# Performance work log

Measured on AMD Instinct MI355X. Metric: run time of the kernel, lower is better.

## Reference

```python
import jax, jax.numpy as jnp
import numpy as np

N_NODES = 50000


def graph_conv(h, src, dst, W, b, num_nodes):
    """GCN-style conv: transform node features, then sum messages over edges.
    h: [N, Din], W: [Din, Dout] -> out: [N, Dout].
    """
    m = (h @ W)[src]                                   # [E, Dout] per-edge messages
    agg = jax.ops.segment_sum(m, dst, num_segments=num_nodes)  # [N, Dout]
    return agg + b


def setup_inputs() -> dict:
    key = jax.random.key(0)
    ks = jax.random.split(key, 8)
    N, E, D = N_NODES, 800000, 128
    s = 1.0 / np.sqrt(2 * D)
    return {
        "node_feature": jax.random.normal(ks[0], (N, D), jnp.float32),
        "H_prev": jax.random.normal(ks[1], (N, D), jnp.float32),
        "edge_index": jax.random.randint(ks[2], (2, E), 0, N, jnp.int32),
        "W_main": jax.random.normal(ks[3], (D, D), jnp.float32) / np.sqrt(D),
        "b_main": jnp.zeros((D,), jnp.float32),
        "W_z": jax.random.normal(ks[4], (2 * D, D), jnp.float32) * s,
        "b_z": jnp.zeros((D,), jnp.float32),
        "W_r": jax.random.normal(ks[5], (2 * D, D), jnp.float32) * s,
        "b_r": jnp.zeros((D,), jnp.float32),
        "W_h": jax.random.normal(ks[6], (2 * D, D), jnp.float32) * s,
        "b_h": jnp.zeros((D,), jnp.float32),
    }


def reference(node_feature, H_prev, edge_index, W_main, b_main,
              W_z, b_z, W_r, b_r, W_h, b_h):
    N = node_feature.shape[0]
    src, dst = edge_index[0], edge_index[1]
    # main message-passing layer + post-layer activation (ReLU)
    X = jax.nn.relu(graph_conv(node_feature, src, dst, W_main, b_main, N))
    # GRU-gated graph convolutions
    cat_zr = jnp.concatenate([X, H_prev], axis=1)       # [N, 2D]
    Z = jax.nn.sigmoid(graph_conv(cat_zr, src, dst, W_z, b_z, N))
    R = jax.nn.sigmoid(graph_conv(cat_zr, src, dst, W_r, b_r, N))
    cat_h = jnp.concatenate([X, R * H_prev], axis=1)
    H_tilde = jnp.tanh(graph_conv(cat_h, src, dst, W_h, b_h, N))
    H_out = Z * H_prev + (1.0 - Z) * H_tilde
    return H_out
```

## Files before the change

kernel.cpp:

```cpp
#include <hip/hip_runtime.h>
#include <hip/hip_fp16.h>
#include <math.h>

typedef _Float16 f16;
typedef f16 f16x2 __attribute__((ext_vector_type(2)));
typedef f16 f16x4 __attribute__((ext_vector_type(4)));
typedef f16 f16x8 __attribute__((ext_vector_type(8)));
typedef float f32x4_t __attribute__((ext_vector_type(4)));

__device__ __forceinline__ float sigmoidf(float x) {
  return 1.0f / (1.0f + __expf(-x));
}

__global__ void zero_ints(int* __restrict__ p, int n) {
  int i = blockIdx.x * blockDim.x + threadIdx.x;
  if (i < n) p[i] = 0;
}

__global__ void count_kernel(const int* __restrict__ dst, int* __restrict__ cnt, int E) {
  int e = blockIdx.x * blockDim.x + threadIdx.x;
  if (e < E) atomicAdd(&cnt[dst[e]], 1);
}

__global__ void scan_kernel(const int* __restrict__ cnt, int* __restrict__ off,
                            int* __restrict__ cur, int n) {
  __shared__ int wsum[16];
  __shared__ int carry_s;
  const int tid = threadIdx.x;
  const int lane = tid & 63, wid = tid >> 6;
  if (tid == 0) carry_s = 0;
  __syncthreads();
  for (int base = 0; base < n; base += 1024) {
    int i = base + tid;
    int v = (i < n) ? cnt[i] : 0;
    int x = v;
    #pragma unroll
    for (int d = 1; d < 64; d <<= 1) {
      int y = __shfl_up(x, d);
      if (lane >= d) x += y;
    }
    if (lane == 63) wsum[wid] = x;
    __syncthreads();
    if (wid == 0) {
      int ws = (lane < 16) ? wsum[lane] : 0;
      #pragma unroll
      for (int d = 1; d < 16; d <<= 1) {
        int y = __shfl_up(ws, d);
        if (lane >= d) ws += y;
      }
      if (lane < 16) wsum[lane] = ws;
    }
    __syncthreads();
    int carry = carry_s;
    int woff = (wid > 0) ? wsum[wid - 1] : 0;
    int incl = x + woff;
    int excl = carry + incl - v;
    if (i < n) { off[i] = excl; cur[i] = excl; }
    __syncthreads();
    if (tid == 1023) carry_s = carry + incl;
    __syncthreads();
  }
  if (threadIdx.x == 0) { off[n] = carry_s; cur[n] = carry_s; }
}

__global__ void fill_kernel(const int* __restrict__ src, const int* __restrict__ dst,
                            int* __restrict__ cur, int* __restrict__ esrc, int E) {
  int e = blockIdx.x * blockDim.x + threadIdx.x;
  if (e < E) {
    int d = dst[e];
    int p = atomicAdd(&cur[d], 1);
    esrc[p] = src[e];
  }
}

__global__ void wtrans_all(const float* __restrict__ Wm, const float* __restrict__ Wz,
                           const float* __restrict__ Wr, const float* __restrict__ Wh,
                           f16* __restrict__ WtM, f16* __restrict__ WtZR,
                           f16* __restrict__ WtH) {
  __shared__ float tile[32][33];
  const float* W;
  f16* O;
  int K;
  switch (blockIdx.z) {
    case 0: W = Wm; O = WtM; K = 128; break;
    case 1: W = Wz; O = WtZR; K = 256; break;
    case 2: W = Wr; O = WtZR + 128 * 256; K = 256; break;
    default: W = Wh; O = WtH; K = 256; break;
  }
  int bk = blockIdx.x * 32, bn = blockIdx.y * 32;
  if (bk >= K) return;
  int tx = threadIdx.x, ty = threadIdx.y;
  #pragma unroll
  for (int i = 0; i < 4; ++i)
    tile[ty + 8 * i][tx] = W[(size_t)(bk + ty + 8 * i) * 128 + bn + tx];
  __syncthreads();
  #pragma unroll
  for (int i = 0; i < 4; ++i)
    O[(size_t)(bn + ty + 8 * i) * K + bk + tx] = (f16)tile[tx][ty + 8 * i];
}

template <int TERMS, int A0F32, int A1F32>
__global__ __launch_bounds__(256) void gemm_mfma(
    const void* __restrict__ A0v, const void* __restrict__ A1v,
    const f16* __restrict__ Wt, f16* __restrict__ C, int ldc, int N) {
  constexpr int KTOT = TERMS * 128;
  __shared__ __align__(16) f16 As[128][72];
  __shared__ __align__(16) f16 Bs[128][72];
  const int tid = threadIdx.x;
  const int l = tid & 63, w = tid >> 6;
  const int wr = (w >> 1) * 64, wc = (w & 1) * 64;
  const int fr = l & 15;
  const int kg = (l >> 4) * 8;
  const int brow = blockIdx.x * 128;
  const int coff = blockIdx.y * 128;

  f32x4_t acc[4][4];
  #pragma unroll
  for (int m = 0; m < 4; ++m)
    #pragma unroll
    for (int n = 0; n < 4; ++n) acc[m][n] = (f32x4_t)0.0f;

  #pragma unroll
  for (int kk = 0; kk < KTOT; kk += 64) {
    const bool sel1 = (TERMS == 2) && (kk >= 128);
    const void* Av = sel1 ? A1v : A0v;
    const bool srcF32 = sel1 ? (A1F32 != 0) : (A0F32 != 0);
    const int klocal = sel1 ? (kk - 128) : kk;

    __syncthreads();
    #pragma unroll
    for (int p = 0; p < 4; ++p) {
      int g = tid + 256 * p;
      int row = g >> 3;
      int kc = (g & 7) * 8;
      int grow = brow + row;
      f16x8 v = {};
      if (grow < N) {
        if (srcF32) {
          const float* Ap = (const float*)Av + (size_t)grow * 128 + klocal + kc;
          float4 u0 = *(const float4*)Ap;
          float4 u1 = *(const float4*)(Ap + 4);
          v[0] = (f16)u0.x; v[1] = (f16)u0.y; v[2] = (f16)u0.z; v[3] = (f16)u0.w;
          v[4] = (f16)u1.x; v[5] = (f16)u1.y; v[6] = (f16)u1.z; v[7] = (f16)u1.w;
        } else {
          v = *(const f16x8*)((const f16*)Av + (size_t)grow * 128 + klocal + kc);
        }
      }
      *(f16x8*)&As[row][kc] = v;
    }
    #pragma unroll
    for (int p = 0; p < 4; ++p) {
      int g = tid + 256 * p;
      int c = g >> 3;
      int kc = (g & 7) * 8;
      *(f16x8*)&Bs[c][kc] = *(const f16x8*)&Wt[(size_t)(coff + c) * KTOT + kk + kc];
    }
    __syncthreads();

    #pragma unroll
    for (int ks = 0; ks < 2; ++ks) {
      f16x8 a[4], b[4];
      #pragma unroll
      for (int m = 0; m < 4; ++m)
        a[m] = *(const f16x8*)&As[wr + m * 16 + fr][ks * 32 + kg];
      #pragma unroll
      for (int n = 0; n < 4; ++n)
        b[n] = *(const f16x8*)&Bs[wc + n * 16 + fr][ks * 32 + kg];
      #pragma unroll
      for (int m = 0; m < 4; ++m)
        #pragma unroll
        for (int n = 0; n < 4; ++n)
          acc[m][n] = __builtin_amdgcn_mfma_f32_16x16x32_f16(a[m], b[n], acc[m][n], 0, 0, 0);
    }
  }

  const int rbase = (l >> 4) * 4;
  if (brow + 128 <= N) {
    #pragma unroll
    for (int m = 0; m < 4; ++m) {
      int row0 = brow + wr + m * 16 + rbase;
      #pragma unroll
      for (int n = 0; n < 4; ++n) {
        int col = coff + wc + n * 16 + fr;
        #pragma unroll
        for (int r = 0; r < 4; ++r)
          C[(size_t)(row0 + r) * ldc + col] = (f16)acc[m][n][r];
      }
    }
  } else {
    #pragma unroll
    for (int m = 0; m < 4; ++m) {
      int row0 = brow + wr + m * 16 + rbase;
      #pragma unroll
      for (int n = 0; n < 4; ++n) {
        int col = coff + wc + n * 16 + fr;
        #pragma unroll
        for (int r = 0; r < 4; ++r)
          if (row0 + r < N) C[(size_t)(row0 + r) * ldc + col] = (f16)acc[m][n][r];
      }
    }
  }
}

__global__ void gather_relu(const f16* __restrict__ T, const int* __restrict__ off,
                            const int* __restrict__ esrc, const float* __restrict__ bias,
                            f16* __restrict__ X, int N) {
  int w = (blockIdx.x * blockDim.x + threadIdx.x) >> 6;
  int lane = threadIdx.x & 63;
  if (w >= N) return;
  int beg = off[w], end = off[w + 1];
  float ax = 0.f, ay = 0.f;
  int j = beg;
  for (; j + 4 <= end; j += 4) {
    int r0 = esrc[j], r1 = esrc[j + 1], r2 = esrc[j + 2], r3 = esrc[j + 3];
    f16x2 v0 = *(const f16x2*)&T[(size_t)r0 * 128 + lane * 2];
    f16x2 v1 = *(const f16x2*)&T[(size_t)r1 * 128 + lane * 2];
    f16x2 v2 = *(const f16x2*)&T[(size_t)r2 * 128 + lane * 2];
    f16x2 v3 = *(const f16x2*)&T[(size_t)r3 * 128 + lane * 2];
    ax += ((float)v0.x + (float)v1.x) + ((float)v2.x + (float)v3.x);
    ay += ((float)v0.y + (float)v1.y) + ((float)v2.y + (float)v3.y);
  }
  for (; j < end; ++j) {
    f16x2 v = *(const f16x2*)&T[(size_t)esrc[j] * 128 + lane * 2];
    ax += (float)v.x; ay += (float)v.y;
  }
  float2 b = *(const float2*)&bias[lane * 2];
  f16x2 o;
  o.x = (f16)fmaxf(ax + b.x, 0.f);
  o.y = (f16)fmaxf(ay + b.y, 0.f);
  *(f16x2*)&X[(size_t)w * 128 + lane * 2] = o;
}

__global__ void gather_zr(const f16* __restrict__ P, const int* __restrict__ off,
                          const int* __restrict__ esrc, const float* __restrict__ bz,
                          const float* __restrict__ br, const float* __restrict__ H,
                          f16* __restrict__ Z, f16* __restrict__ G, int N) {
  int w = (blockIdx.x * blockDim.x + threadIdx.x) >> 6;
  int lane = threadIdx.x & 63;
  if (w >= N) return;
  int beg = off[w], end = off[w + 1];
  float a0 = 0.f, a1 = 0.f, a2 = 0.f, a3 = 0.f;
  int j = beg;
  for (; j + 4 <= end; j += 4) {
    int r0 = esrc[j], r1 = esrc[j + 1], r2 = esrc[j + 2], r3 = esrc[j + 3];
    f16x4 v0 = *(const f16x4*)&P[(size_t)r0 * 256 + lane * 4];
    f16x4 v1 = *(const f16x4*)&P[(size_t)r1 * 256 + lane * 4];
    f16x4 v2 = *(const f16x4*)&P[(size_t)r2 * 256 + lane * 4];
    f16x4 v3 = *(const f16x4*)&P[(size_t)r3 * 256 + lane * 4];
    a0 += ((float)v0.x + (float)v1.x) + ((float)v2.x + (float)v3.x);
    a1 += ((float)v0.y + (float)v1.y) + ((float)v2.y + (float)v3.y);
    a2 += ((float)v0.z + (float)v1.z) + ((float)v2.z + (float)v3.z);
    a3 += ((float)v0.w + (float)v1.w) + ((float)v2.w + (float)v3.w);
  }
  for (; j < end; ++j) {
    f16x4 v = *(const f16x4*)&P[(size_t)esrc[j] * 256 + lane * 4];
    a0 += (float)v.x; a1 += (float)v.y; a2 += (float)v.z; a3 += (float)v.w;
  }
  if (lane < 32) {
    int c = lane * 4;
    float4 b = *(const float4*)&bz[c];
    f16x4 o;
    o.x = (f16)sigmoidf(a0 + b.x);
    o.y = (f16)sigmoidf(a1 + b.y);
    o.z = (f16)sigmoidf(a2 + b.z);
    o.w = (f16)sigmoidf(a3 + b.w);
    *(f16x4*)&Z[(size_t)w * 128 + c] = o;
  } else {
    int c = (lane - 32) * 4;
    float4 b = *(const float4*)&br[c];
    float4 h = *(const float4*)&H[(size_t)w * 128 + c];
    f16x4 o;
    o.x = (f16)(sigmoidf(a0 + b.x) * h.x);
    o.y = (f16)(sigmoidf(a1 + b.y) * h.y);
    o.z = (f16)(sigmoidf(a2 + b.z) * h.z);
    o.w = (f16)(sigmoidf(a3 + b.w) * h.w);
    *(f16x4*)&G[(size_t)w * 128 + c] = o;
  }
}

__global__ void gather_out(const f16* __restrict__ T, const int* __restrict__ off,
                           const int* __restrict__ esrc, const float* __restrict__ bh,
                           const f16* __restrict__ Z, const float* __restrict__ H,
                           float* __restrict__ out, int N) {
  int w = (blockIdx.x * blockDim.x + threadIdx.x) >> 6;
  int lane = threadIdx.x & 63;
  if (w >= N) return;
  int beg = off[w], end = off[w + 1];
  float ax = 0.f, ay = 0.f;
  int j = beg;
  for (; j + 4 <= end; j += 4) {
    int r0 = esrc[j], r1 = esrc[j + 1], r2 = esrc[j + 2], r3 = esrc[j + 3];
    f16x2 v0 = *(const f16x2*)&T[(size_t)r0 * 128 + lane * 2];
    f16x2 v1 = *(const f16x2*)&T[(size_t)r1 * 128 + lane * 2];
    f16x2 v2 = *(const f16x2*)&T[(size_t)r2 * 128 + lane * 2];
    f16x2 v3 = *(const f16x2*)&T[(size_t)r3 * 128 + lane * 2];
    ax += ((float)v0.x + (float)v1.x) + ((float)v2.x + (float)v3.x);
    ay += ((float)v0.y + (float)v1.y) + ((float)v2.y + (float)v3.y);
  }
  for (; j < end; ++j) {
    f16x2 v = *(const f16x2*)&T[(size_t)esrc[j] * 128 + lane * 2];
    ax += (float)v.x; ay += (float)v.y;
  }
  float2 b = *(const float2*)&bh[lane * 2];
  float h0 = tanhf(ax + b.x), h1 = tanhf(ay + b.y);
  size_t q = (size_t)w * 128 + lane * 2;
  f16x2 zv = *(const f16x2*)&Z[q];
  float2 h = *(const float2*)&H[q];
  float z0 = (float)zv.x, z1 = (float)zv.y;
  float2 o;
  o.x = z0 * h.x + (1.0f - z0) * h0;
  o.y = z1 * h.y + (1.0f - z1) * h1;
  *(float2*)&out[q] = o;
}


extern "C" void kernel_launch(void* const* d_in, const int* in_sizes, int n_in,
                              void* d_out, int out_size, void* d_ws, size_t ws_size,
                              hipStream_t stream) {
  const float* nf = (const float*)d_in[0];
  const float* H  = (const float*)d_in[1];
  const int*   ei = (const int*)d_in[2];
  const float* Wm = (const float*)d_in[3];
  const float* bm = (const float*)d_in[4];
  const float* Wz = (const float*)d_in[5];
  const float* bz = (const float*)d_in[6];
  const float* Wr = (const float*)d_in[7];
  const float* br = (const float*)d_in[8];
  const float* Wh = (const float*)d_in[9];
  const float* bh = (const float*)d_in[10];
  float* out = (float*)d_out;

  const int N = in_sizes[0] / 128;
  const int E = in_sizes[2] / 2;
  const int* src = ei;
  const int* dst = ei + E;

  char* ws = (char*)d_ws;
  size_t o = 0;
  auto alloc = [&](size_t bytes) {
    char* p = ws + o;
    o = (o + bytes + 511) & ~(size_t)511;
    return p;
  };
  int* cnt    = (int*)alloc((size_t)N * 4);
  int* off    = (int*)alloc((size_t)(N + 1) * 4);
  int* cur    = (int*)alloc((size_t)(N + 1) * 4);
  int* esrc   = (int*)alloc((size_t)E * 4);
  f16* WtM    = (f16*)alloc((size_t)128 * 128 * 2);
  f16* WtZR   = (f16*)alloc((size_t)256 * 256 * 2);
  f16* WtH    = (f16*)alloc((size_t)128 * 256 * 2);
  f16* Tm     = (f16*)alloc((size_t)N * 128 * 2);
  f16* Pzr    = (f16*)alloc((size_t)N * 256 * 2);
  f16* Th     = (f16*)alloc((size_t)N * 128 * 2);
  f16* X      = (f16*)alloc((size_t)N * 128 * 2);
  f16* G      = (f16*)alloc((size_t)N * 128 * 2);
  f16* Zh     = (f16*)alloc((size_t)N * 128 * 2);

  zero_ints<<<(N + 255) / 256, 256, 0, stream>>>(cnt, N);
  count_kernel<<<(E + 255) / 256, 256, 0, stream>>>(dst, cnt, E);
  scan_kernel<<<1, 1024, 0, stream>>>(cnt, off, cur, N);
  fill_kernel<<<(E + 255) / 256, 256, 0, stream>>>(src, dst, cur, esrc, E);

  wtrans_all<<<dim3(8, 4, 4), dim3(32, 8), 0, stream>>>(Wm, Wz, Wr, Wh, WtM, WtZR, WtH);

  const int gblk = (N * 64 + 255) / 256;
  const int mblk = (N + 127) / 128;

  gemm_mfma<1, 1, 0><<<dim3(mblk, 1), 256, 0, stream>>>(nf, nullptr, WtM, Tm, 128, N);
  gather_relu<<<gblk, 256, 0, stream>>>(Tm, off, esrc, bm, X, N);

  gemm_mfma<2, 0, 1><<<dim3(mblk, 2), 256, 0, stream>>>(X, H, WtZR, Pzr, 256, N);
  gather_zr<<<gblk, 256, 0, stream>>>(Pzr, off, esrc, bz, br, H, Zh, G, N);

  gemm_mfma<2, 0, 0><<<dim3(mblk, 1), 256, 0, stream>>>(X, G, WtH, Th, 128, N);
  gather_out<<<gblk, 256, 0, stream>>>(Th, off, esrc, bh, Zh, H, out, N);
}
```

Before: 334.4 us.

## Aggregate before transforming, fuse activations into GEMM epilogues, parallelize CSR scan

Uses linearity to reorder each graph conv from transform-then-gather to gather-then-transform, so neighbor sums run on packed f16 inputs and the bias and activations (ReLU, sigmoid, tanh and the GRU blend) move into the MFMA GEMM epilogues. The separate gather kernels with fused activations go away, and the buffers for node features, Z and the output are aliased to reuse memory. The single-block CSR prefix scan becomes a three-kernel multi-block scan, and edge sources are stored as pre-shifted byte offsets to save address arithmetic. The cost is an extra pack kernel that converts node features and H to f16, plus ordering constraints from the buffer aliasing; there are also small rounding differences because sums are now taken before the matmul.

```diff
diff --git a/kernel.cpp b/kernel.cpp
--- a/kernel.cpp
+++ b/kernel.cpp
@@ -22,55 +22,84 @@
   if (e < E) atomicAdd(&cnt[dst[e]], 1);
 }
 
-__global__ void scan_kernel(const int* __restrict__ cnt, int* __restrict__ off,
-                            int* __restrict__ cur, int n) {
+__global__ __launch_bounds__(1024) void scan_local(const int* __restrict__ cnt,
+                                                   int* __restrict__ off,
+                                                   int* __restrict__ psum, int n) {
   __shared__ int wsum[16];
-  __shared__ int carry_s;
-  const int tid = threadIdx.x;
-  const int lane = tid & 63, wid = tid >> 6;
-  if (tid == 0) carry_s = 0;
-  __syncthreads();
-  for (int base = 0; base < n; base += 1024) {
-    int i = base + tid;
-    int v = (i < n) ? cnt[i] : 0;
-    int x = v;
-    #pragma unroll
-    for (int d = 1; d < 64; d <<= 1) {
-      int y = __shfl_up(x, d);
-      if (lane >= d) x += y;
-    }
-    if (lane == 63) wsum[wid] = x;
-    __syncthreads();
-    if (wid == 0) {
-      int ws = (lane < 16) ? wsum[lane] : 0;
-      #pragma unroll
-      for (int d = 1; d < 16; d <<= 1) {
-        int y = __shfl_up(ws, d);
-        if (lane >= d) ws += y;
-      }
-      if (lane < 16) wsum[lane] = ws;
-    }
-    __syncthreads();
-    int carry = carry_s;
-    int woff = (wid > 0) ? wsum[wid - 1] : 0;
-    int incl = x + woff;
-    int excl = carry + incl - v;
-    if (i < n) { off[i] = excl; cur[i] = excl; }
-    __syncthreads();
-    if (tid == 1023) carry_s = carry + incl;
-    __syncthreads();
-  }
-  if (threadIdx.x == 0) { off[n] = carry_s; cur[n] = carry_s; }
+  const int tid = threadIdx.x, lane = tid & 63, wid = tid >> 6;
+  int i = blockIdx.x * 1024 + tid;
+  int v = (i < n) ? cnt[i] : 0;
+  int x = v;
+  #pragma unroll
+  for (int d = 1; d < 64; d <<= 1) { int y = __shfl_up(x, d); if (lane >= d) x += y; }
+  if (lane == 63) wsum[wid] = x;
+  __syncthreads();
+  if (wid == 0) {
+    int ws = (lane < 16) ? wsum[lane] : 0;
+    #pragma unroll
+    for (int d = 1; d < 16; d <<= 1) { int y = __shfl_up(ws, d); if (lane >= d) ws += y; }
+    if (lane < 16) wsum[lane] = ws;
+  }
+  __syncthreads();
+  int excl = x - v + (wid ? wsum[wid - 1] : 0);
+  if (i < n) off[i] = excl;
+  if (tid == 1023) psum[blockIdx.x] = wsum[15];
+}
+
+__global__ __launch_bounds__(1024) void scan_carry(int* __restrict__ psum,
+                                                   int* __restrict__ off,
+                                                   int* __restrict__ cur, int nb, int n) {
+  __shared__ int wsum[16];
+  const int tid = threadIdx.x, lane = tid & 63, wid = tid >> 6;
+  int v = (tid < nb) ? psum[tid] : 0;
+  int x = v;
+  #pragma unroll
+  for (int d = 1; d < 64; d <<= 1) { int y = __shfl_up(x, d); if (lane >= d) x += y; }
+  if (lane == 63) wsum[wid] = x;
+  __syncthreads();
+  if (wid == 0) {
+    int ws = (lane < 16) ? wsum[lane] : 0;
+    #pragma unroll
+    for (int d = 1; d < 16; d <<= 1) { int y = __shfl_up(ws, d); if (lane >= d) ws += y; }
+    if (lane < 16) wsum[lane] = ws;
+  }
+  __syncthreads();
+  int excl = x - v + (wid ? wsum[wid - 1] : 0);
+  if (tid < nb) psum[tid] = excl;
+  if (tid == 1023) { off[n] = wsum[15]; cur[n] = wsum[15]; }
+}
+
+__global__ __launch_bounds__(1024) void scan_add(int* __restrict__ off, int* __restrict__ cur,
+                                                 const int* __restrict__ psum, int n) {
+  int i = blockIdx.x * 1024 + threadIdx.x;
+  if (i < n) {
+    int t = off[i] + psum[blockIdx.x];
+    off[i] = t;
+    cur[i] = t;
+  }
 }
 
 __global__ void fill_kernel(const int* __restrict__ src, const int* __restrict__ dst,
-                            int* __restrict__ cur, int* __restrict__ esrc, int E) {
+                            int* __restrict__ cur, int* __restrict__ eoff, int E) {
   int e = blockIdx.x * blockDim.x + threadIdx.x;
   if (e < E) {
     int d = dst[e];
     int p = atomicAdd(&cur[d], 1);
-    esrc[p] = src[e];
-  }
+    eoff[p] = src[e] << 8;
+  }
+}
+
+__global__ void pack_nfh(const float* __restrict__ nf, const float* __restrict__ H,
+                         f16* __restrict__ P0, int N) {
+  int gid = blockIdx.x * blockDim.x + threadIdx.x;
+  int w = gid >> 6;
+  if (w >= N) return;
+  int lane = threadIdx.x & 63;
+  const float* S = (lane < 32) ? nf : H;
+  int c = (lane & 31) * 4;
+  float4 u = *(const float4*)&S[(size_t)w * 128 + c];
+  f16x4 o = {(f16)u.x, (f16)u.y, (f16)u.z, (f16)u.w};
+  *(f16x4*)&P0[(size_t)w * 256 + (lane < 32 ? 0 : 128) + c] = o;
 }
 
 __global__ void wtrans_all(const float* __restrict__ Wm, const float* __restrict__ Wz,
@@ -99,10 +128,68 @@
     O[(size_t)(bn + ty + 8 * i) * K + bk + tx] = (f16)tile[tx][ty + 8 * i];
 }
 
-template <int TERMS, int A0F32, int A1F32>
+template <int COLS>
+__global__ __launch_bounds__(256) void gather(const f16* __restrict__ P,
+                                              const int* __restrict__ off,
+                                              const int* __restrict__ eoff,
+                                              f16* __restrict__ O, int N) {
+  int gid = blockIdx.x * blockDim.x + threadIdx.x;
+  int w = __builtin_amdgcn_readfirstlane(gid >> 6);
+  if (w >= N) return;
+  const int lane = threadIdx.x & 63;
+  const int beg = off[w], end = off[w + 1];
+  const char* base = (const char*)P;
+  int j = beg;
+  if constexpr (COLS == 256) {
+    const int lb = lane * 8;
+    float a0 = 0.f, a1 = 0.f, a2 = 0.f, a3 = 0.f;
+    for (; j + 8 <= end; j += 8) {
+      f16x4 v[8];
+      #pragma unroll
+      for (int u = 0; u < 8; ++u) {
+        int bo = (eoff[j + u] << 1) + lb;
+        v[u] = *(const f16x4*)(base + bo);
+      }
+      #pragma unroll
+      for (int u = 0; u < 8; ++u) {
+        a0 += (float)v[u].x; a1 += (float)v[u].y;
+        a2 += (float)v[u].z; a3 += (float)v[u].w;
+      }
+    }
+    for (; j < end; ++j) {
+      int bo = (eoff[j] << 1) + lb;
+      f16x4 v = *(const f16x4*)(base + bo);
+      a0 += (float)v.x; a1 += (float)v.y; a2 += (float)v.z; a3 += (float)v.w;
+    }
+    f16x4 o = {(f16)a0, (f16)a1, (f16)a2, (f16)a3};
+    *(f16x4*)&O[(size_t)w * 256 + lane * 4] = o;
+  } else {
+    const int lb = lane * 4;
+    float a0 = 0.f, a1 = 0.f;
+    for (; j + 8 <= end; j += 8) {
+      f16x2 v[8];
+      #pragma unroll
+      for (int u = 0; u < 8; ++u)
+        v[u] = *(const f16x2*)(base + eoff[j + u] + lb);
+      #pragma unroll
+      for (int u = 0; u < 8; ++u) { a0 += (float)v[u].x; a1 += (float)v[u].y; }
+    }
+    for (; j < end; ++j) {
+      f16x2 v = *(const f16x2*)(base + eoff[j] + lb);
+      a0 += (float)v.x; a1 += (float)v.y;
+    }
+    f16x2 o = {(f16)a0, (f16)a1};
+    *(f16x2*)&O[(size_t)w * 128 + lane * 2] = o;
+  }
+}
+
+template <int TERMS, int EPI>
 __global__ __launch_bounds__(256) void gemm_mfma(
-    const void* __restrict__ A0v, const void* __restrict__ A1v,
-    const f16* __restrict__ Wt, f16* __restrict__ C, int ldc, int N) {
+    const f16* __restrict__ A0, int lda0, const f16* __restrict__ A1, int lda1,
+    const f16* __restrict__ Wt,
+    const float* __restrict__ b0, const float* __restrict__ b1,
+    const float* __restrict__ H, const f16* __restrict__ Zh,
+    f16* __restrict__ O0, f16* __restrict__ O1, float* __restrict__ Ofp, int N) {
   constexpr int KTOT = TERMS * 128;
   __shared__ __align__(16) f16 As[128][72];
   __shared__ __align__(16) f16 Bs[128][72];
@@ -123,9 +210,9 @@
   #pragma unroll
   for (int kk = 0; kk < KTOT; kk += 64) {
     const bool sel1 = (TERMS == 2) && (kk >= 128);
-    const void* Av = sel1 ? A1v : A0v;
-    const bool srcF32 = sel1 ? (A1F32 != 0) : (A0F32 != 0);
-    const int klocal = sel1 ? (kk - 128) : kk;
+    const f16* __restrict__ A = sel1 ? A1 : A0;
+    const int lda = sel1 ? lda1 : lda0;
+    const int klocal = kk & 127;
 
     __syncthreads();
     #pragma unroll
@@ -135,17 +222,7 @@
       int kc = (g & 7) * 8;
       int grow = brow + row;
       f16x8 v = {};
-      if (grow < N) {
-        if (srcF32) {
-          const float* Ap = (const float*)Av + (size_t)grow * 128 + klocal + kc;
-          float4 u0 = *(const float4*)Ap;
-          float4 u1 = *(const float4*)(Ap + 4);
-          v[0] = (f16)u0.x; v[1] = (f16)u0.y; v[2] = (f16)u0.z; v[3] = (f16)u0.w;
-          v[4] = (f16)u1.x; v[5] = (f16)u1.y; v[6] = (f16)u1.z; v[7] = (f16)u1.w;
-        } else {
-          v = *(const f16x8*)((const f16*)Av + (size_t)grow * 128 + klocal + kc);
-        }
-      }
+      if (grow < N) v = *(const f16x8*)&A[(size_t)grow * lda + klocal + kc];
       *(f16x8*)&As[row][kc] = v;
     }
     #pragma unroll
@@ -175,142 +252,56 @@
   }
 
   const int rbase = (l >> 4) * 4;
-  if (brow + 128 <= N) {
-    #pragma unroll
-    for (int m = 0; m < 4; ++m) {
-      int row0 = brow + wr + m * 16 + rbase;
-      #pragma unroll
-      for (int n = 0; n < 4; ++n) {
-        int col = coff + wc + n * 16 + fr;
+  #pragma unroll
+  for (int m = 0; m < 4; ++m) {
+    int row0 = brow + wr + m * 16 + rbase;
+    #pragma unroll
+    for (int n = 0; n < 4; ++n) {
+      int colL = wc + n * 16 + fr;
+      if (EPI == 0) {
+        float bias = b0[colL];
         #pragma unroll
-        for (int r = 0; r < 4; ++r)
-          C[(size_t)(row0 + r) * ldc + col] = (f16)acc[m][n][r];
+        for (int r = 0; r < 4; ++r) {
+          int row = row0 + r;
+          if (row < N)
+            O0[(size_t)row * 128 + colL] = (f16)fmaxf(acc[m][n][r] + bias, 0.f);
+        }
+      } else if (EPI == 1) {
+        if (coff == 0) {
+          float bias = b0[colL];
+          #pragma unroll
+          for (int r = 0; r < 4; ++r) {
+            int row = row0 + r;
+            if (row < N)
+              O0[(size_t)row * 128 + colL] = (f16)sigmoidf(acc[m][n][r] + bias);
+          }
+        } else {
+          float bias = b1[colL];
+          #pragma unroll
+          for (int r = 0; r < 4; ++r) {
+            int row = row0 + r;
+            if (row < N) {
+              float g = sigmoidf(acc[m][n][r] + bias) * H[(size_t)row * 128 + colL];
+              O1[(size_t)row * 128 + colL] = (f16)g;
+            }
+          }
+        }
+      } else {
+        float bias = b0[colL];
+        #pragma unroll
+        for (int r = 0; r < 4; ++r) {
+          int row = row0 + r;
+          if (row < N) {
+            size_t q = (size_t)row * 128 + colL;
+            float ht = tanhf(acc[m][n][r] + bias);
+            float z = (float)Zh[q];
+            float h = H[q];
+            Ofp[q] = z * h + (1.0f - z) * ht;
+          }
+        }
       }
     }
-  } else {
-    #pragma unroll
-    for (int m = 0; m < 4; ++m) {
-      int row0 = brow + wr + m * 16 + rbase;
-      #pragma unroll
-      for (int n = 0; n < 4; ++n) {
-        int col = coff + wc + n * 16 + fr;
-        #pragma unroll
-        for (int r = 0; r < 4; ++r)
-          if (row0 + r < N) C[(size_t)(row0 + r) * ldc + col] = (f16)acc[m][n][r];
-      }
-    }
-  }
-}
-
-__global__ void gather_relu(const f16* __restrict__ T, const int* __restrict__ off,
-                            const int* __restrict__ esrc, const float* __restrict__ bias,
-                            f16* __restrict__ X, int N) {
-  int w = (blockIdx.x * blockDim.x + threadIdx.x) >> 6;
-  int lane = threadIdx.x & 63;
-  if (w >= N) return;
-  int beg = off[w], end = off[w + 1];
-  float ax = 0.f, ay = 0.f;
-  int j = beg;
-  for (; j + 4 <= end; j += 4) {
-    int r0 = esrc[j], r1 = esrc[j + 1], r2 = esrc[j + 2], r3 = esrc[j + 3];
-    f16x2 v0 = *(const f16x2*)&T[(size_t)r0 * 128 + lane * 2];
-    f16x2 v1 = *(const f16x2*)&T[(size_t)r1 * 128 + lane * 2];
-    f16x2 v2 = *(const f16x2*)&T[(size_t)r2 * 128 + lane * 2];
-    f16x2 v3 = *(const f16x2*)&T[(size_t)r3 * 128 + lane * 2];
-    ax += ((float)v0.x + (float)v1.x) + ((float)v2.x + (float)v3.x);
-    ay += ((float)v0.y + (float)v1.y) + ((float)v2.y + (float)v3.y);
-  }
-  for (; j < end; ++j) {
-    f16x2 v = *(const f16x2*)&T[(size_t)esrc[j] * 128 + lane * 2];
-    ax += (float)v.x; ay += (float)v.y;
-  }
-  float2 b = *(const float2*)&bias[lane * 2];
-  f16x2 o;
-  o.x = (f16)fmaxf(ax + b.x, 0.f);
-  o.y = (f16)fmaxf(ay + b.y, 0.f);
-  *(f16x2*)&X[(size_t)w * 128 + lane * 2] = o;
-}
-
-__global__ void gather_zr(const f16* __restrict__ P, const int* __restrict__ off,
-                          const int* __restrict__ esrc, const float* __restrict__ bz,
-                          const float* __restrict__ br, const float* __restrict__ H,
-                          f16* __restrict__ Z, f16* __restrict__ G, int N) {
-  int w = (blockIdx.x * blockDim.x + threadIdx.x) >> 6;
-  int lane = threadIdx.x & 63;
-  if (w >= N) return;
-  int beg = off[w], end = off[w + 1];
-  float a0 = 0.f, a1 = 0.f, a2 = 0.f, a3 = 0.f;
-  int j = beg;
-  for (; j + 4 <= end; j += 4) {
-    int r0 = esrc[j], r1 = esrc[j + 1], r2 = esrc[j + 2], r3 = esrc[j + 3];
-    f16x4 v0 = *(const f16x4*)&P[(size_t)r0 * 256 + lane * 4];
-    f16x4 v1 = *(const f16x4*)&P[(size_t)r1 * 256 + lane * 4];
-    f16x4 v2 = *(const f16x4*)&P[(size_t)r2 * 256 + lane * 4];
-    f16x4 v3 = *(const f16x4*)&P[(size_t)r3 * 256 + lane * 4];
-    a0 += ((float)v0.x + (float)v1.x) + ((float)v2.x + (float)v3.x);
-    a1 += ((float)v0.y + (float)v1.y) + ((float)v2.y + (float)v3.y);
-    a2 += ((float)v0.z + (float)v1.z) + ((float)v2.z + (float)v3.z);
-    a3 += ((float)v0.w + (float)v1.w) + ((float)v2.w + (float)v3.w);
-  }
-  for (; j < end; ++j) {
-    f16x4 v = *(const f16x4*)&P[(size_t)esrc[j] * 256 + lane * 4];
-    a0 += (float)v.x; a1 += (float)v.y; a2 += (float)v.z; a3 += (float)v.w;
-  }
-  if (lane < 32) {
-    int c = lane * 4;
-    float4 b = *(const float4*)&bz[c];
-    f16x4 o;
-    o.x = (f16)sigmoidf(a0 + b.x);
-    o.y = (f16)sigmoidf(a1 + b.y);
-    o.z = (f16)sigmoidf(a2 + b.z);
-    o.w = (f16)sigmoidf(a3 + b.w);
-    *(f16x4*)&Z[(size_t)w * 128 + c] = o;
-  } else {
-    int c = (lane - 32) * 4;
-    float4 b = *(const float4*)&br[c];
-    float4 h = *(const float4*)&H[(size_t)w * 128 + c];
-    f16x4 o;
-    o.x = (f16)(sigmoidf(a0 + b.x) * h.x);
-    o.y = (f16)(sigmoidf(a1 + b.y) * h.y);
-    o.z = (f16)(sigmoidf(a2 + b.z) * h.z);
-    o.w = (f16)(sigmoidf(a3 + b.w) * h.w);
-    *(f16x4*)&G[(size_t)w * 128 + c] = o;
-  }
-}
-
-__global__ void gather_out(const f16* __restrict__ T, const int* __restrict__ off,
-                           const int* __restrict__ esrc, const float* __restrict__ bh,
-                           const f16* __restrict__ Z, const float* __restrict__ H,
-                           float* __restrict__ out, int N) {
-  int w = (blockIdx.x * blockDim.x + threadIdx.x) >> 6;
-  int lane = threadIdx.x & 63;
-  if (w >= N) return;
-  int beg = off[w], end = off[w + 1];
-  float ax = 0.f, ay = 0.f;
-  int j = beg;
-  for (; j + 4 <= end; j += 4) {
-    int r0 = esrc[j], r1 = esrc[j + 1], r2 = esrc[j + 2], r3 = esrc[j + 3];
-    f16x2 v0 = *(const f16x2*)&T[(size_t)r0 * 128 + lane * 2];
-    f16x2 v1 = *(const f16x2*)&T[(size_t)r1 * 128 + lane * 2];
-    f16x2 v2 = *(const f16x2*)&T[(size_t)r2 * 128 + lane * 2];
-    f16x2 v3 = *(const f16x2*)&T[(size_t)r3 * 128 + lane * 2];
-    ax += ((float)v0.x + (float)v1.x) + ((float)v2.x + (float)v3.x);
-    ay += ((float)v0.y + (float)v1.y) + ((float)v2.y + (float)v3.y);
-  }
-  for (; j < end; ++j) {
-    f16x2 v = *(const f16x2*)&T[(size_t)esrc[j] * 128 + lane * 2];
-    ax += (float)v.x; ay += (float)v.y;
-  }
-  float2 b = *(const float2*)&bh[lane * 2];
-  float h0 = tanhf(ax + b.x), h1 = tanhf(ay + b.y);
-  size_t q = (size_t)w * 128 + lane * 2;
-  f16x2 zv = *(const f16x2*)&Z[q];
-  float2 h = *(const float2*)&H[q];
-  float z0 = (float)zv.x, z1 = (float)zv.y;
-  float2 o;
-  o.x = z0 * h.x + (1.0f - z0) * h0;
-  o.y = z1 * h.y + (1.0f - z1) * h1;
-  *(float2*)&out[q] = o;
+  }
 }
 
 
@@ -342,36 +333,48 @@
     o = (o + bytes + 511) & ~(size_t)511;
     return p;
   };
+  const int nb = (N + 1023) / 1024;
   int* cnt    = (int*)alloc((size_t)N * 4);
   int* off    = (int*)alloc((size_t)(N + 1) * 4);
   int* cur    = (int*)alloc((size_t)(N + 1) * 4);
-  int* esrc   = (int*)alloc((size_t)E * 4);
+  int* eoff   = (int*)alloc((size_t)E * 4);
+  int* psum   = (int*)alloc((size_t)nb * 4);
   f16* WtM    = (f16*)alloc((size_t)128 * 128 * 2);
   f16* WtZR   = (f16*)alloc((size_t)256 * 256 * 2);
   f16* WtH    = (f16*)alloc((size_t)128 * 256 * 2);
-  f16* Tm     = (f16*)alloc((size_t)N * 128 * 2);
-  f16* Pzr    = (f16*)alloc((size_t)N * 256 * 2);
-  f16* Th     = (f16*)alloc((size_t)N * 128 * 2);
+  f16* P0     = (f16*)alloc((size_t)N * 256 * 2);
   f16* X      = (f16*)alloc((size_t)N * 128 * 2);
+  f16* AX     = (f16*)alloc((size_t)N * 128 * 2);
   f16* G      = (f16*)alloc((size_t)N * 128 * 2);
-  f16* Zh     = (f16*)alloc((size_t)N * 128 * 2);
+  f16* AP0    = (f16*)d_out;
+  f16* Zh     = X;
+  f16* AG     = P0;
 
   zero_ints<<<(N + 255) / 256, 256, 0, stream>>>(cnt, N);
   count_kernel<<<(E + 255) / 256, 256, 0, stream>>>(dst, cnt, E);
-  scan_kernel<<<1, 1024, 0, stream>>>(cnt, off, cur, N);
-  fill_kernel<<<(E + 255) / 256, 256, 0, stream>>>(src, dst, cur, esrc, E);
+  scan_local<<<nb, 1024, 0, stream>>>(cnt, off, psum, N);
+  scan_carry<<<1, 1024, 0, stream>>>(psum, off, cur, nb, N);
+  scan_add<<<nb, 1024, 0, stream>>>(off, cur, psum, N);
+  fill_kernel<<<(E + 255) / 256, 256, 0, stream>>>(src, dst, cur, eoff, E);
 
   wtrans_all<<<dim3(8, 4, 4), dim3(32, 8), 0, stream>>>(Wm, Wz, Wr, Wh, WtM, WtZR, WtH);
-
   const int gblk = (N * 64 + 255) / 256;
+  pack_nfh<<<gblk, 256, 0, stream>>>(nf, H, P0, N);
+
   const int mblk = (N + 127) / 128;
 
-  gemm_mfma<1, 1, 0><<<dim3(mblk, 1), 256, 0, stream>>>(nf, nullptr, WtM, Tm, 128, N);
-  gather_relu<<<gblk, 256, 0, stream>>>(Tm, off, esrc, bm, X, N);
-
-  gemm_mfma<2, 0, 1><<<dim3(mblk, 2), 256, 0, stream>>>(X, H, WtZR, Pzr, 256, N);
-  gather_zr<<<gblk, 256, 0, stream>>>(Pzr, off, esrc, bz, br, H, Zh, G, N);
-
-  gemm_mfma<2, 0, 0><<<dim3(mblk, 1), 256, 0, stream>>>(X, G, WtH, Th, 128, N);
-  gather_out<<<gblk, 256, 0, stream>>>(Th, off, esrc, bh, Zh, H, out, N);
-}
+  gather<256><<<gblk, 256, 0, stream>>>(P0, off, eoff, AP0, N);
+
+  gemm_mfma<1, 0><<<dim3(mblk, 1), 256, 0, stream>>>(
+      AP0, 256, nullptr, 0, WtM, bm, nullptr, nullptr, nullptr, X, nullptr, nullptr, N);
+
+  gather<128><<<gblk, 256, 0, stream>>>(X, off, eoff, AX, N);
+
+  gemm_mfma<2, 1><<<dim3(mblk, 2), 256, 0, stream>>>(
+      AX, 128, AP0 + 128, 256, WtZR, bz, br, H, nullptr, Zh, G, nullptr, N);
+
+  gather<128><<<gblk, 256, 0, stream>>>(G, off, eoff, AG, N);
+
+  gemm_mfma<2, 2><<<dim3(mblk, 1), 256, 0, stream>>>(
+      AX, 128, AG, 128, WtH, bh, nullptr, H, Zh, nullptr, nullptr, out, N);
+}
```

Result: no change. 329.9 us (-1.4%).
